# Performance work log

Hardware: AMD Instinct MI355X
Metric: run time of the kernel (lower is better)

## Reference

```python
import jax, jax.numpy as jnp
import numpy as np
import math

B, L, D, K = 16, 8192, 256, 320
BN_EPS = 1e-5


def setup_inputs() -> dict:
    key = jax.random.key(0)
    k1, k2, k3, k4 = jax.random.split(key, 4)
    x = jax.random.normal(k1, (B, L, D), dtype=jnp.float32)
    bn_weight = 1.0 + 0.1 * jax.random.normal(k2, (D,), dtype=jnp.float32)
    bn_bias = 0.1 * jax.random.normal(k3, (D,), dtype=jnp.float32)
    # xavier_uniform for Embedding(numCodes, codeDim)
    a = math.sqrt(6.0 / (K + D))
    codebook = jax.random.uniform(k4, (K, D), minval=-a, maxval=a, dtype=jnp.float32)
    return {"x": x, "bn_weight": bn_weight, "bn_bias": bn_bias, "codebook": codebook}


def batchnorm1d(x, weight, bias):
    # BatchNorm1d in training mode: stats over (batch, length) per channel,
    # biased variance for normalization (matches torch).
    mean = jnp.mean(x, axis=(0, 1))
    var = jnp.var(x, axis=(0, 1))
    return (x - mean) * jax.lax.rsqrt(var + BN_EPS) * weight + bias


def reference(x, bn_weight, bn_bias, codebook):
    xb = batchnorm1d(x, bn_weight, bn_bias)            # [B, L, D]
    flat = xb.reshape(-1, D)                           # [B*L, D]
    # squared euclidean distance (same argmin as torch.cdist)
    d2 = (jnp.sum(flat * flat, axis=-1, keepdims=True)
          - 2.0 * flat @ codebook.T
          + jnp.sum(codebook * codebook, axis=-1))     # [B*L, K]
    indices = jnp.argmin(d2, axis=-1)                  # [B*L]
    codes = codebook[indices].reshape(B, L, D)         # gather nearest codes
    return codes, indices.reshape(B, L, 1)
```

## Files before the change

kernel.cpp:

```cpp
#include <hip/hip_runtime.h>
#include <hip/hip_bf16.h>

#define NROW 131072
#define D 256
#define K 320
#define BN_EPS 1e-5f
#define FIXSCALE 16777216.0f

typedef _Float16 half8 __attribute__((ext_vector_type(8)));
typedef float f32x4 __attribute__((ext_vector_type(4)));


__global__ __launch_bounds__(256) void k_zero(unsigned long long* __restrict__ acc) {
  acc[threadIdx.x] = 0ull;
  acc[256 + threadIdx.x] = 0ull;
}

__global__ __launch_bounds__(256) void k_stats_partial(const float* __restrict__ x,
                                                       unsigned long long* __restrict__ acc) {
  const int d = threadIdx.x;
  const int blk = blockIdx.x;
  const float* p = x + (size_t)blk * 256 * D + d;
  float s = 0.f, q = 0.f;
  #pragma unroll 4
  for (int r = 0; r < 256; ++r) {
    float v = p[(size_t)r * D];
    s += v;
    q = fmaf(v, v, q);
  }
  long long si = llrintf(s * FIXSCALE);
  long long qi = llrintf(q * FIXSCALE);
  atomicAdd(&acc[d],       (unsigned long long)si);
  atomicAdd(&acc[256 + d], (unsigned long long)qi);
}

__global__ __launch_bounds__(256) void k_stats_final(const unsigned long long* __restrict__ acc,
                                                     const float* __restrict__ cb,
                                                     float* __restrict__ meanb,
                                                     float* __restrict__ rsb,
                                                     float* __restrict__ cnorm) {
  const int t = threadIdx.x;
  if (blockIdx.x == 0) {
    double s = (double)(long long)acc[t]       / (double)FIXSCALE;
    double q = (double)(long long)acc[256 + t] / (double)FIXSCALE;
    double mean = s / (double)NROW;
    double var  = q / (double)NROW - mean * mean;
    meanb[t] = (float)mean;
    rsb[t]   = (float)(1.0 / sqrt(var + (double)BN_EPS));
  } else {
    for (int code = t; code < K; code += 256) {
      const float* c = cb + (size_t)code * D;
      float s = 0.f;
      for (int dd = 0; dd < D; ++dd) s = fmaf(c[dd], c[dd], s);
      cnorm[code] = s;
    }
  }
}

__global__ __launch_bounds__(64) void k_cbprep(const float* __restrict__ cb,
                                               _Float16* __restrict__ cbx) {
  const int nt = blockIdx.x;
  const int ks = blockIdx.y;
  const int l  = threadIdx.x;
  const int code = nt * 16 + (l & 15);
  const int d0 = ks * 32 + (l >> 4) * 8;
  const float* src = cb + (size_t)code * D + d0;
  const size_t bh = ((size_t)(nt * 2 + 0) * 8 + ks) * 512 + l * 8;
  const size_t bl = ((size_t)(nt * 2 + 1) * 8 + ks) * 512 + l * 8;
  #pragma unroll
  for (int j = 0; j < 8; ++j) {
    float v = src[j];
    _Float16 h = (_Float16)v;
    _Float16 lo = (_Float16)(v - (float)h);
    cbx[bh + j] = h;
    cbx[bl + j] = lo;
  }
}

__global__ __launch_bounds__(256) void k_main(const float* __restrict__ x,
                                              const float* __restrict__ w,
                                              const float* __restrict__ bias,
                                              const float* __restrict__ cb,
                                              const float* __restrict__ meanb,
                                              const float* __restrict__ rsb,
                                              const float* __restrict__ cnorm,
                                              const _Float16* __restrict__ cbx,
                                              float* __restrict__ out) {
  __shared__ _Float16 Bbuf[2][8192];
  __shared__ float sxs[64];
  __shared__ int bsel[64];

  const int t = threadIdx.x;
  const int lane = t & 63;
  const int wv = t >> 6;
  const int c15 = lane & 15;
  const int g = lane >> 4;
  const int row0 = (int)blockIdx.x * 64;

  float4 s0, s1, s2, s3;
  const char* stg_src = (const char*)cbx + (size_t)t * 16;
#define ISSUE(c) {                                                  \
    const char* p_ = stg_src + (size_t)(c) * 16384;                 \
    s0 = *(const float4*)(p_);                                      \
    s1 = *(const float4*)(p_ + 4096);                               \
    s2 = *(const float4*)(p_ + 8192);                               \
    s3 = *(const float4*)(p_ + 12288);                              \
  }
#define WRITE(b) {                                                  \
    char* q_ = (char*)Bbuf[(b)] + t * 16;                           \
    *(float4*)(q_)         = s0;                                    \
    *(float4*)(q_ + 4096)  = s1;                                    \
    *(float4*)(q_ + 8192)  = s2;                                    \
    *(float4*)(q_ + 12288) = s3;                                    \
  }

  ISSUE(0);

  half8 ah[8], al[8];
  float accq = 0.f;
  {
    const int arow = row0 + wv * 16 + c15;
    const int dbase = g * 8;
    const float* xp = x + (size_t)arow * D + dbase;
    #pragma unroll
    for (int ks = 0; ks < 8; ++ks) {
      const int d0 = dbase + ks * 32;
      float4 xa = *(const float4*)(xp + ks * 32);
      float4 xb2 = *(const float4*)(xp + ks * 32 + 4);
      float4 m0 = *(const float4*)(meanb + d0);
      float4 m1 = *(const float4*)(meanb + d0 + 4);
      float4 r0 = *(const float4*)(rsb + d0);
      float4 r1 = *(const float4*)(rsb + d0 + 4);
      float4 w0 = *(const float4*)(w + d0);
      float4 w1 = *(const float4*)(w + d0 + 4);
      float4 b0 = *(const float4*)(bias + d0);
      float4 b1 = *(const float4*)(bias + d0 + 4);
      float o0 = ((xa.x - m0.x) * r0.x) * w0.x + b0.x;
      float o1 = ((xa.y - m0.y) * r0.y) * w0.y + b0.y;
      float o2 = ((xa.z - m0.z) * r0.z) * w0.z + b0.z;
      float o3 = ((xa.w - m0.w) * r0.w) * w0.w + b0.w;
      float o4 = ((xb2.x - m1.x) * r1.x) * w1.x + b1.x;
      float o5 = ((xb2.y - m1.y) * r1.y) * w1.y + b1.y;
      float o6 = ((xb2.z - m1.z) * r1.z) * w1.z + b1.z;
      float o7 = ((xb2.w - m1.w) * r1.w) * w1.w + b1.w;
      accq = fmaf(o0, o0, accq); accq = fmaf(o1, o1, accq);
      accq = fmaf(o2, o2, accq); accq = fmaf(o3, o3, accq);
      accq = fmaf(o4, o4, accq); accq = fmaf(o5, o5, accq);
      accq = fmaf(o6, o6, accq); accq = fmaf(o7, o7, accq);
      _Float16 h;
      h = (_Float16)o0; ah[ks][0] = h; al[ks][0] = (_Float16)(o0 - (float)h);
      h = (_Float16)o1; ah[ks][1] = h; al[ks][1] = (_Float16)(o1 - (float)h);
      h = (_Float16)o2; ah[ks][2] = h; al[ks][2] = (_Float16)(o2 - (float)h);
      h = (_Float16)o3; ah[ks][3] = h; al[ks][3] = (_Float16)(o3 - (float)h);
      h = (_Float16)o4; ah[ks][4] = h; al[ks][4] = (_Float16)(o4 - (float)h);
      h = (_Float16)o5; ah[ks][5] = h; al[ks][5] = (_Float16)(o5 - (float)h);
      h = (_Float16)o6; ah[ks][6] = h; al[ks][6] = (_Float16)(o6 - (float)h);
      h = (_Float16)o7; ah[ks][7] = h; al[ks][7] = (_Float16)(o7 - (float)h);
    }
  }

  WRITE(0);
  ISSUE(1);

  {
    float v1 = accq + __shfl_xor(accq, 16);
    float sxrow = v1 + __shfl_xor(v1, 32);
    if (lane < 16) sxs[wv * 16 + lane] = sxrow;
  }
  __syncthreads();

  float bv[4];
  int   bix[4];
  #pragma unroll
  for (int r = 0; r < 4; ++r) { bv[r] = 3.4e38f; bix[r] = 0x7fffffff; }

  float sxr[4];
  #pragma unroll
  for (int r = 0; r < 4; ++r) sxr[r] = sxs[wv * 16 + g * 4 + r];

  for (int c = 0; c < 20; ++c) {
    if (c + 1 < 20) WRITE((c + 1) & 1);
    if (c + 2 < 20) ISSUE(c + 2);

    {
      const _Float16* bb = Bbuf[c & 1] + lane * 8;
      f32x4 acc = (f32x4){0.f, 0.f, 0.f, 0.f};
      #pragma unroll
      for (int ks = 0; ks < 8; ++ks) {
        half8 bh = *(const half8*)(bb + ks * 512);
        half8 bl = *(const half8*)(bb + 4096 + ks * 512);
        acc = __builtin_amdgcn_mfma_f32_16x16x32_f16(ah[ks], bh, acc, 0, 0, 0);
        acc = __builtin_amdgcn_mfma_f32_16x16x32_f16(ah[ks], bl, acc, 0, 0, 0);
        acc = __builtin_amdgcn_mfma_f32_16x16x32_f16(al[ks], bh, acc, 0, 0, 0);
      }
      const int code = c * 16 + c15;
      const float cn = cnorm[code];
      #pragma unroll
      for (int r = 0; r < 4; ++r) {
        const float d2 = (sxr[r] - 2.0f * acc[r]) + cn;
        if (d2 < bv[r] || (d2 == bv[r] && code < bix[r])) { bv[r] = d2; bix[r] = code; }
      }
    }
    if (c < 19) __syncthreads();
  }

  #pragma unroll
  for (int off = 8; off >= 1; off >>= 1) {
    #pragma unroll
    for (int r = 0; r < 4; ++r) {
      const float ov = __shfl_xor(bv[r], off);
      const int   oi = __shfl_xor(bix[r], off);
      if (ov < bv[r] || (ov == bv[r] && oi < bix[r])) { bv[r] = ov; bix[r] = oi; }
    }
  }
  if (c15 == 0) {
    #pragma unroll
    for (int r = 0; r < 4; ++r) {
      const int row = wv * 16 + g * 4 + r;
      bsel[row] = bix[r];
      out[(size_t)NROW * D + row0 + row] = (float)bix[r];
    }
  }
  __syncthreads();

  {
    const int lr = t >> 2;
    const int q = t & 3;
    const int code = bsel[lr];
    const float* cp = cb + (size_t)code * D;
    float* op = out + (size_t)(row0 + lr) * D;
    #pragma unroll
    for (int e = 0; e < 16; ++e) {
      *(float4*)(op + e * 16 + q * 4) = *(const float4*)(cp + e * 16 + q * 4);
    }
  }
#undef ISSUE
#undef WRITE
}

extern "C" void kernel_launch(void* const* d_in, const int* in_sizes, int n_in,
                              void* d_out, int out_size, void* d_ws, size_t ws_size,
                              hipStream_t stream) {
  const float* x    = (const float*)d_in[0];
  const float* w    = (const float*)d_in[1];
  const float* bias = (const float*)d_in[2];
  const float* cb   = (const float*)d_in[3];
  float* out = (float*)d_out;

  unsigned long long* acc = (unsigned long long*)d_ws;
  float* meanb = (float*)((char*)d_ws + 4096);
  float* rsb   = meanb + 256;
  float* cnorm = rsb + 256;
  _Float16* cbx = (_Float16*)((char*)d_ws + 8192);

  k_zero<<<1, 256, 0, stream>>>(acc);
  k_cbprep<<<dim3(20, 8), 64, 0, stream>>>(cb, cbx);
  k_stats_partial<<<512, 256, 0, stream>>>(x, acc);
  k_stats_final<<<2, 256, 0, stream>>>(acc, cb, meanb, rsb, cnorm);
  k_main<<<NROW / 64, 256, 0, stream>>>(x, w, bias, cb, meanb, rsb, cnorm, cbx, out);
}
```

Baseline: 146.4 us.

## Stage codebook via direct global-to-LDS loads and fold accumulator zeroing into prep

Replaces the register-staged codebook double buffer (global load to registers, then an LDS write) with global_load_lds intrinsics that write straight into the alternate LDS buffer. This frees staging registers and removes the LDS store instructions from the loop. The prefetch distance drops from two chunks to one. The separate zeroing kernel is merged into k_cbprep as an extra block, saving one launch. The hidden loop body must wait on vmcnt and sync before reading each buffer, otherwise the loads can race.

```diff
diff --git a/kernel.cpp b/kernel.cpp
--- a/kernel.cpp
+++ b/kernel.cpp
@@ -9,12 +9,9 @@
 
 typedef _Float16 half8 __attribute__((ext_vector_type(8)));
 typedef float f32x4 __attribute__((ext_vector_type(4)));
-
-
-__global__ __launch_bounds__(256) void k_zero(unsigned long long* __restrict__ acc) {
-  acc[threadIdx.x] = 0ull;
-  acc[256 + threadIdx.x] = 0ull;
-}
+typedef __attribute__((address_space(3))) unsigned int lds_u32;
+typedef __attribute__((address_space(1))) const unsigned int g_u32;
+
 
 __global__ __launch_bounds__(256) void k_stats_partial(const float* __restrict__ x,
                                                        unsigned long long* __restrict__ acc) {
@@ -58,10 +55,17 @@
 }
 
 __global__ __launch_bounds__(64) void k_cbprep(const float* __restrict__ cb,
-                                               _Float16* __restrict__ cbx) {
-  const int nt = blockIdx.x;
-  const int ks = blockIdx.y;
-  const int l  = threadIdx.x;
+                                               _Float16* __restrict__ cbx,
+                                               unsigned long long* __restrict__ acc) {
+  const int b = blockIdx.x;
+  const int l = threadIdx.x;
+  if (b == 160) {
+    #pragma unroll
+    for (int j = 0; j < 8; ++j) acc[j * 64 + l] = 0ull;
+    return;
+  }
+  const int nt = b >> 3;
+  const int ks = b & 7;
   const int code = nt * 16 + (l & 15);
   const int d0 = ks * 32 + (l >> 4) * 8;
   const float* src = cb + (size_t)code * D + d0;
@@ -97,21 +101,14 @@
   const int g = lane >> 4;
   const int row0 = (int)blockIdx.x * 64;
 
-  float4 s0, s1, s2, s3;
-  const char* stg_src = (const char*)cbx + (size_t)t * 16;
-#define ISSUE(c) {                                                  \
-    const char* p_ = stg_src + (size_t)(c) * 16384;                 \
-    s0 = *(const float4*)(p_);                                      \
-    s1 = *(const float4*)(p_ + 4096);                               \
-    s2 = *(const float4*)(p_ + 8192);                               \
-    s3 = *(const float4*)(p_ + 12288);                              \
-  }
-#define WRITE(b) {                                                  \
-    char* q_ = (char*)Bbuf[(b)] + t * 16;                           \
-    *(float4*)(q_)         = s0;                                    \
-    *(float4*)(q_ + 4096)  = s1;                                    \
-    *(float4*)(q_ + 8192)  = s2;                                    \
-    *(float4*)(q_ + 12288) = s3;                                    \
+#define ISSUE(c) {                                                            \
+    const char* gp_ = (const char*)cbx + (size_t)(c) * 16384 + wv * 4096      \
+                      + (size_t)lane * 16;                                    \
+    _Float16* lp_ = Bbuf[(c) & 1] + wv * 2048 + lane * 8;                     \
+    __builtin_amdgcn_global_load_lds((g_u32*)(gp_),        (lds_u32*)(lp_),         16, 0, 0); \
+    __builtin_amdgcn_global_load_lds((g_u32*)(gp_ + 1024), (lds_u32*)(lp_ + 512),   16, 0, 0); \
+    __builtin_amdgcn_global_load_lds((g_u32*)(gp_ + 2048), (lds_u32*)(lp_ + 1024),  16, 0, 0); \
+    __builtin_amdgcn_global_load_lds((g_u32*)(gp_ + 3072), (lds_u32*)(lp_ + 1536),  16, 0, 0); \
   }
 
   ISSUE(0);
@@ -159,9 +156,6 @@
     }
   }
 
-  WRITE(0);
-  ISSUE(1);
-
   {
     float v1 = accq + __shfl_xor(accq, 16);
     float sxrow = v1 + __shfl_xor(v1, 32);
@@ -179,8 +173,7 @@
   for (int r = 0; r < 4; ++r) sxr[r] = sxs[wv * 16 + g * 4 + r];
 
   for (int c = 0; c < 20; ++c) {
-    if (c + 1 < 20) WRITE((c + 1) & 1);
-    if (c + 2 < 20) ISSUE(c + 2);
+    if (c + 1 < 20) ISSUE(c + 1);
 
     {
       const _Float16* bb = Bbuf[c & 1] + lane * 8;
@@ -235,7 +228,6 @@
     }
   }
 #undef ISSUE
-#undef WRITE
 }
 
 extern "C" void kernel_launch(void* const* d_in, const int* in_sizes, int n_in,
@@ -253,8 +245,7 @@
   float* cnorm = rsb + 256;
   _Float16* cbx = (_Float16*)((char*)d_ws + 8192);
 
-  k_zero<<<1, 256, 0, stream>>>(acc);
-  k_cbprep<<<dim3(20, 8), 64, 0, stream>>>(cb, cbx);
+  k_cbprep<<<161, 64, 0, stream>>>(cb, cbx, acc);
   k_stats_partial<<<512, 256, 0, stream>>>(x, acc);
   k_stats_final<<<2, 256, 0, stream>>>(acc, cb, meanb, rsb, cnorm);
   k_main<<<NROW / 64, 256, 0, stream>>>(x, w, bias, cb, meanb, rsb, cnorm, cbx, out);
```

Result: slower. 171.9 us (+17.5%).
